# Performance work log

Measured on AMD Instinct MI355X. Metric: run time of the kernel, lower is better.

Reference implementation:

```python
import jax, jax.numpy as jnp
import numpy as np

SEQ, B, I, H = 4096, 256, 64, 64

def setup_inputs() -> dict:
    key = jax.random.key(0)
    k1, k2, k3, k4, k5 = jax.random.split(key, 5)
    s = 1.0 / np.sqrt(H)  # torch nn.RNN init: U(-1/sqrt(H), 1/sqrt(H))
    return {
        "input": jax.random.normal(k1, (SEQ, B, I), dtype=jnp.float32),
        "w_ih": jax.random.uniform(k2, (H, I), jnp.float32, -s, s),
        "w_hh": jax.random.uniform(k3, (H, H), jnp.float32, -s, s),
        "b_ih": jax.random.uniform(k4, (H,), jnp.float32, -s, s),
        "b_hh": jax.random.uniform(k5, (H,), jnp.float32, -s, s),
    }

def reference(input, w_ih, w_hh, b_ih, b_hh):
    # Vanilla tanh RNN: h_t = tanh(x_t @ W_ih^T + b_ih + h_{t-1} @ W_hh^T + b_hh)
    # Precompute input projection for all timesteps in one big GEMM.
    x_proj = jnp.einsum('sbi,hi->sbh', input, w_ih) + b_ih + b_hh  # [S,B,H]
    h0 = jnp.zeros((input.shape[1], w_hh.shape[0]), dtype=input.dtype)

    def step(h, xp):
        h_new = jnp.tanh(xp + h @ w_hh.T)
        return h_new, h_new

    _, out = jax.lax.scan(step, h0, x_proj)  # out: [S,B,H]
    return out.reshape(-1, w_hh.shape[0])
```

## Files before the change

kernel.cpp:

```cpp
#include <hip/hip_runtime.h>

#define SEQL 4096
#define NB   256
#define NH   64

__device__ __forceinline__ float rl(float v, int lane) {
  return __builtin_bit_cast(float,
      __builtin_amdgcn_readlane(__builtin_bit_cast(int, v), lane));
}

__global__ __launch_bounds__(64) void xproj(const float* __restrict__ x,
                                            const float* __restrict__ w_ih,
                                            const float* __restrict__ b_ih,
                                            const float* __restrict__ b_hh,
                                            float* __restrict__ dst) {
  const int i = threadIdx.x;
  const size_t rbase = (size_t)blockIdx.x * 256;

  float4 w[16];
  const float4* wr = (const float4*)(w_ih + (size_t)i * NH);
#pragma unroll
  for (int k = 0; k < 16; ++k) w[k] = wr[k];
  const float bias = b_ih[i] + b_hh[i];

  const float4* xg = (const float4*)(x + rbase * NH) + i;
  float* og = dst + rbase * NH + i;

  float4 v = *xg;

#define XROWS()                                               \
  {                                                           \
    _Pragma("unroll")                                         \
    for (int r = 0; r < 4; ++r) {                             \
      float a = bias;                                         \
      _Pragma("unroll")                                       \
      for (int m = 0; m < 16; ++m) {                          \
        float4 wv = w[m];                                     \
        a = fmaf(wv.x, rl(v.x, 16 * r + m), a);               \
        a = fmaf(wv.y, rl(v.y, 16 * r + m), a);               \
        a = fmaf(wv.z, rl(v.z, 16 * r + m), a);               \
        a = fmaf(wv.w, rl(v.w, 16 * r + m), a);               \
      }                                                       \
      og[r * NH] = a;                                         \
    }                                                         \
    og += 4 * NH;                                             \
  }

#pragma unroll 1
  for (int g = 0; g < 63; ++g) {
    float4 vn = xg[64];
    xg += 64;
    XROWS();
    v = vn;
  }
  XROWS();
#undef XROWS
}

__device__ __forceinline__ void rec_run(const float* __restrict__ w_hh,
                                        const float* __restrict__ xp,
                                        float* __restrict__ out, int b, int i) {
  float4 w[16];
  const float4* wr = (const float4*)(w_hh + (size_t)i * NH);
#pragma unroll
  for (int k = 0; k < 16; ++k) w[k] = wr[k];

  const size_t step = (size_t)NB * NH;
  const float* px = xp + (size_t)b * NH + i;
  float* po = out + (size_t)b * NH + i;

  float xq0 = px[0];
  float xq1 = px[step];
  float xq2 = px[2 * step];
  float xq3 = px[3 * step];
  px += 4 * step;

  float hn = 0.f;

#define RSTEP(XQ, PF)                                            \
  {                                                              \
    float a0 = XQ, a1 = 0.f, a2 = 0.f, a3 = 0.f;                 \
    if (PF) { XQ = px[0]; px += step; }     \
    _Pragma("unroll")                                            \
    for (int m = 0; m < 16; ++m) {                               \
      float4 wv = w[m];                                          \
      a0 = fmaf(wv.x, rl(hn, 4 * m + 0), a0);                    \
      a1 = fmaf(wv.y, rl(hn, 4 * m + 1), a1);                    \
      a2 = fmaf(wv.z, rl(hn, 4 * m + 2), a2);                    \
      a3 = fmaf(wv.w, rl(hn, 4 * m + 3), a3);                    \
    }                                                            \
    float z = (a0 + a1) + (a2 + a3);                             \
    z = fminf(15.f, fmaxf(-15.f, z));                            \
    float e2 = __builtin_amdgcn_exp2f(z * 2.885390081777927f);   \
    hn = (e2 - 1.f) * __builtin_amdgcn_rcpf(e2 + 1.f);           \
    po[0] = hn;                                                  \
    po += step;                                                  \
  }

#pragma unroll 1
  for (int s = 0; s < SEQL - 4; s += 4) {
    RSTEP(xq0, 1) RSTEP(xq1, 1) RSTEP(xq2, 1) RSTEP(xq3, 1)
  }
  RSTEP(xq0, 0) RSTEP(xq1, 0) RSTEP(xq2, 0) RSTEP(xq3, 0)
#undef RSTEP
}

__global__ __launch_bounds__(64) void rnn_rec_split(const float* __restrict__ w_hh,
                                                    const float* __restrict__ xp,
                                                    float* __restrict__ out) {
  rec_run(w_hh, xp, out, blockIdx.x, threadIdx.x);
}

__global__ __launch_bounds__(64) void rnn_rec_inpl(const float* __restrict__ w_hh,
                                                   float* __restrict__ out) {
  rec_run(w_hh, out, out, blockIdx.x, threadIdx.x);
}

extern "C" void kernel_launch(void* const* d_in, const int* in_sizes, int n_in,
                              void* d_out, int out_size, void* d_ws, size_t ws_size,
                              hipStream_t stream) {
  const float* x    = (const float*)d_in[0];
  const float* w_ih = (const float*)d_in[1];
  const float* w_hh = (const float*)d_in[2];
  const float* b_ih = (const float*)d_in[3];
  const float* b_hh = (const float*)d_in[4];
  float* out = (float*)d_out;

  const size_t need = (size_t)SEQL * NB * NH * sizeof(float);
  if (d_ws && ws_size >= need) {
    float* xpbuf = (float*)d_ws;
    xproj<<<dim3(4096), dim3(64), 0, stream>>>(x, w_ih, b_ih, b_hh, xpbuf);
    rnn_rec_split<<<dim3(NB), dim3(64), 0, stream>>>(w_hh, xpbuf, out);
  } else {
    xproj<<<dim3(4096), dim3(64), 0, stream>>>(x, w_ih, b_ih, b_hh, out);
    rnn_rec_inpl<<<dim3(NB), dim3(64), 0, stream>>>(w_hh, out);
  }
}
```

Before: 1.644 ms.

## Register-tile input projection GEMM and batch readlanes before recurrence FMAs

The input projection kernel changes from one column per lane with a readlane broadcast per FMA to 256-thread blocks in which each thread computes an 8x8 register tile from float4 loads of x and w_ih, with vectorized stores. In the recurrence, all 64 readlanes of the hidden state are gathered into a register array first, and a sched_barrier separates them from the FMA chain. The aim is to cut readlane overhead in the GEMM and let the scalar broadcasts issue back to back off the serial critical path. The cost is much higher register pressure (a 64-float accumulator tile plus operands, and 64 extra registers per step), and w_ih is now re-read uncoalesced by each thread.

```diff
diff --git a/kernel.cpp b/kernel.cpp
--- a/kernel.cpp
+++ b/kernel.cpp
@@ -9,53 +9,80 @@
       __builtin_amdgcn_readlane(__builtin_bit_cast(int, v), lane));
 }
 
-__global__ __launch_bounds__(64) void xproj(const float* __restrict__ x,
-                                            const float* __restrict__ w_ih,
-                                            const float* __restrict__ b_ih,
-                                            const float* __restrict__ b_hh,
-                                            float* __restrict__ dst) {
-  const int i = threadIdx.x;
-  const size_t rbase = (size_t)blockIdx.x * 256;
+__global__ __launch_bounds__(256) void xproj(const float* __restrict__ x,
+                                             const float* __restrict__ w_ih,
+                                             const float* __restrict__ b_ih,
+                                             const float* __restrict__ b_hh,
+                                             float* __restrict__ dst) {
+  const int t  = threadIdx.x;
+  const int tc = t & 7;
+  const int tr = t >> 3;
+  const size_t rbase = (size_t)blockIdx.x * 256 + (size_t)tr * 8;
+  const int c0 = tc * 8;
 
-  float4 w[16];
-  const float4* wr = (const float4*)(w_ih + (size_t)i * NH);
+  float acc[8][8];
 #pragma unroll
-  for (int k = 0; k < 16; ++k) w[k] = wr[k];
-  const float bias = b_ih[i] + b_hh[i];
-
-  const float4* xg = (const float4*)(x + rbase * NH) + i;
-  float* og = dst + rbase * NH + i;
-
-  float4 v = *xg;
-
-#define XROWS()                                               \
-  {                                                           \
-    _Pragma("unroll")                                         \
-    for (int r = 0; r < 4; ++r) {                             \
-      float a = bias;                                         \
-      _Pragma("unroll")                                       \
-      for (int m = 0; m < 16; ++m) {                          \
-        float4 wv = w[m];                                     \
-        a = fmaf(wv.x, rl(v.x, 16 * r + m), a);               \
-        a = fmaf(wv.y, rl(v.y, 16 * r + m), a);               \
-        a = fmaf(wv.z, rl(v.z, 16 * r + m), a);               \
-        a = fmaf(wv.w, rl(v.w, 16 * r + m), a);               \
-      }                                                       \
-      og[r * NH] = a;                                         \
-    }                                                         \
-    og += 4 * NH;                                             \
+  for (int cc = 0; cc < 8; ++cc) {
+    float b = b_ih[c0 + cc] + b_hh[c0 + cc];
+#pragma unroll
+    for (int rr = 0; rr < 8; ++rr) acc[rr][cc] = b;
   }
 
-#pragma unroll 1
-  for (int g = 0; g < 63; ++g) {
-    float4 vn = xg[64];
-    xg += 64;
-    XROWS();
-    v = vn;
+  const float4* xb4 = (const float4*)(x + rbase * NH);
+  const float4* wb4 = (const float4*)(w_ih + (size_t)c0 * NH);
+
+#pragma unroll
+  for (int kq = 0; kq < 16; ++kq) {
+    float4 wq[8], xq[8];
+#pragma unroll
+    for (int cc = 0; cc < 8; ++cc) wq[cc] = wb4[cc * 16 + kq];
+#pragma unroll
+    for (int rr = 0; rr < 8; ++rr) xq[rr] = xb4[rr * 16 + kq];
+#pragma unroll
+    for (int rr = 0; rr < 8; ++rr)
+#pragma unroll
+      for (int cc = 0; cc < 8; ++cc) {
+        float a = acc[rr][cc];
+        a = fmaf(xq[rr].x, wq[cc].x, a);
+        a = fmaf(xq[rr].y, wq[cc].y, a);
+        a = fmaf(xq[rr].z, wq[cc].z, a);
+        a = fmaf(xq[rr].w, wq[cc].w, a);
+        acc[rr][cc] = a;
+      }
   }
-  XROWS();
-#undef XROWS
+
+  float* ob = dst + rbase * NH + c0;
+#pragma unroll
+  for (int rr = 0; rr < 8; ++rr) {
+    *(float4*)(ob + rr * NH)     = make_float4(acc[rr][0], acc[rr][1], acc[rr][2], acc[rr][3]);
+    *(float4*)(ob + rr * NH + 4) = make_float4(acc[rr][4], acc[rr][5], acc[rr][6], acc[rr][7]);
+  }
 }
+
+#define RSTEP(XQ, PF)                                            \
+  {                                                              \
+    float xcur = XQ;                                             \
+    if (PF) { XQ = px[0]; px += step; }     \
+    float hb[64];                                                \
+    _Pragma("unroll")                                            \
+    for (int j = 0; j < 64; ++j) hb[j] = rl(hn, j);              \
+    __builtin_amdgcn_sched_barrier(0);                           \
+    float a0 = xcur, a1 = 0.f, a2 = 0.f, a3 = 0.f;               \
+    _Pragma("unroll")                                            \
+    for (int m = 0; m < 16; ++m) {                               \
+      float4 wv = w[m];                                          \
+      a0 = fmaf(wv.x, hb[4 * m + 0], a0);                        \
+      a1 = fmaf(wv.y, hb[4 * m + 1], a1);                        \
+      a2 = fmaf(wv.z, hb[4 * m + 2], a2);                        \
+      a3 = fmaf(wv.w, hb[4 * m + 3], a3);                        \
+    }                                                            \
+    float z = (a0 + a1) + (a2 + a3);                             \
+    z = fminf(15.f, fmaxf(-15.f, z));                            \
+    float e2 = __builtin_amdgcn_exp2f(z * 2.885390081777927f);   \
+    hn = (e2 - 1.f) * __builtin_amdgcn_rcpf(e2 + 1.f);           \
+    po[0] = hn;                                                  \
+    po += step;                                                  \
+  }
 
 __device__ __forceinline__ void rec_run(const float* __restrict__ w_hh,
                                         const float* __restrict__ xp,
@@ -77,33 +104,13 @@
 
   float hn = 0.f;
 
-#define RSTEP(XQ, PF)                                            \
-  {                                                              \
-    float a0 = XQ, a1 = 0.f, a2 = 0.f, a3 = 0.f;                 \
-    if (PF) { XQ = px[0]; px += step; }     \
-    _Pragma("unroll")                                            \
-    for (int m = 0; m < 16; ++m) {                               \
-      float4 wv = w[m];                                          \
-      a0 = fmaf(wv.x, rl(hn, 4 * m + 0), a0);                    \
-      a1 = fmaf(wv.y, rl(hn, 4 * m + 1), a1);                    \
-      a2 = fmaf(wv.z, rl(hn, 4 * m + 2), a2);                    \
-      a3 = fmaf(wv.w, rl(hn, 4 * m + 3), a3);                    \
-    }                                                            \
-    float z = (a0 + a1) + (a2 + a3);                             \
-    z = fminf(15.f, fmaxf(-15.f, z));                            \
-    float e2 = __builtin_amdgcn_exp2f(z * 2.885390081777927f);   \
-    hn = (e2 - 1.f) * __builtin_amdgcn_rcpf(e2 + 1.f);           \
-    po[0] = hn;                                                  \
-    po += step;                                                  \
-  }
-
 #pragma unroll 1
   for (int s = 0; s < SEQL - 4; s += 4) {
     RSTEP(xq0, 1) RSTEP(xq1, 1) RSTEP(xq2, 1) RSTEP(xq3, 1)
   }
   RSTEP(xq0, 0) RSTEP(xq1, 0) RSTEP(xq2, 0) RSTEP(xq3, 0)
+}
 #undef RSTEP
-}
 
 __global__ __launch_bounds__(64) void rnn_rec_split(const float* __restrict__ w_hh,
                                                     const float* __restrict__ xp,
@@ -129,10 +136,10 @@
   const size_t need = (size_t)SEQL * NB * NH * sizeof(float);
   if (d_ws && ws_size >= need) {
     float* xpbuf = (float*)d_ws;
-    xproj<<<dim3(4096), dim3(64), 0, stream>>>(x, w_ih, b_ih, b_hh, xpbuf);
+    xproj<<<dim3(4096), dim3(256), 0, stream>>>(x, w_ih, b_ih, b_hh, xpbuf);
     rnn_rec_split<<<dim3(NB), dim3(64), 0, stream>>>(w_hh, xpbuf, out);
   } else {
-    xproj<<<dim3(4096), dim3(64), 0, stream>>>(x, w_ih, b_ih, b_hh, out);
+    xproj<<<dim3(4096), dim3(256), 0, stream>>>(x, w_ih, b_ih, b_hh, out);
     rnn_rec_inpl<<<dim3(NB), dim3(64), 0, stream>>>(w_hh, out);
   }
 }
```

New measurement: 1.688 ms. 2.7% more time.
